# Kernel optimization log

Measured on AMD Instinct MI355X. Metric: run time of the kernel, lower is better.

Reference implementation:

```python
import math
import jax, jax.numpy as jnp
import numpy as np

B = 8
NUM_POINTS = 4096
LATENT = 512
HID = 512
AD = 128
R1, R2, R_ATT = 1.0, 1.5, 0.2
EPS = 1e-5
SQRT_D = math.sqrt(AD)


def _fibonacci_sphere_points(n, radius):
    if n <= 0:
        return np.zeros((0, 3), np.float32)
    i = np.arange(n, dtype=np.float32)
    phi = (1 + 5 ** 0.5) / 2
    theta = 2 * math.pi * i / phi
    z = 1.0 - 2.0 * (i + 0.5) / n
    r_xy = np.sqrt(np.maximum(1.0 - z * z, 0.0))
    return (radius * np.stack((r_xy * np.cos(theta), r_xy * np.sin(theta), z), axis=-1)).astype(np.float32)


def _make_template():
    n_shell = NUM_POINTS - 1
    area_ratio = R1 ** 2 / (R1 ** 2 + R2 ** 2)
    n1 = max(1, round(n_shell * area_ratio))
    n2 = n_shell - n1
    if n2 == 0:
        n1, n2 = n1 - 1, 1
    t1 = _fibonacci_sphere_points(n1, R1)
    t2 = _fibonacci_sphere_points(n2, R2)
    return jnp.asarray(np.concatenate([np.zeros((1, 3), np.float32), t1, t2], axis=0))


def setup_inputs() -> dict:
    key = jax.random.key(0)
    ks = iter(jax.random.split(key, 64))
    d = {}
    d['z'] = jax.random.normal(next(ks), (B, LATENT), jnp.float32)
    d['template'] = _make_template()
    d['wq'] = jax.random.normal(next(ks), (AD, 3), jnp.float32) * 0.1
    d['wk'] = jax.random.normal(next(ks), (AD, 3), jnp.float32) * 0.1
    d['wv'] = jax.random.normal(next(ks), (AD, 3), jnp.float32) * 0.1
    in_dims = [LATENT + 3, LATENT + 3 + AD, LATENT + 3 + AD]
    for s, in_dim in enumerate(in_dims):
        d[f's{s}_w1'] = jax.random.normal(next(ks), (HID, in_dim), jnp.float32) * (1.0 / math.sqrt(in_dim))
        d[f's{s}_b1'] = jnp.zeros((HID,), jnp.float32)
        d[f's{s}_g1'] = jnp.ones((HID,), jnp.float32)
        d[f's{s}_be1'] = jnp.zeros((HID,), jnp.float32)
        d[f's{s}_w2'] = jax.random.normal(next(ks), (HID, HID), jnp.float32) * (1.0 / math.sqrt(HID))
        d[f's{s}_b2'] = jnp.zeros((HID,), jnp.float32)
        d[f's{s}_g2'] = jnp.ones((HID,), jnp.float32)
        d[f's{s}_be2'] = jnp.zeros((HID,), jnp.float32)
        d[f's{s}_w3'] = jax.random.normal(next(ks), (3, HID), jnp.float32) * (1.0 / math.sqrt(HID))
        d[f's{s}_b3'] = jnp.zeros((3,), jnp.float32)
    return d


def _bn_relu(x, gamma, beta):
    # BatchNorm1d in training mode over channel dim of (B, N, C): stats over (B, N)
    mean = jnp.mean(x, axis=(0, 1))
    var = jnp.var(x, axis=(0, 1))
    xn = (x - mean) * jax.lax.rsqrt(var + EPS)
    return jax.nn.relu(xn * gamma + beta)


def _stage(x, w1, b1, g1, be1, w2, b2, g2, be2, w3, b3):
    h = _bn_relu(x @ w1.T + b1, g1, be1)
    h = _bn_relu(h @ w2.T + b2, g2, be2)
    return h @ w3.T + b3


def _local_attention(coords, wq, wk, wv):
    Q = coords @ wq.T  # (B, N, AD)
    K = coords @ wk.T
    V = coords @ wv.T
    sq = jnp.sum(coords * coords, axis=-1)  # (B, N)
    D2 = sq[:, :, None] + sq[:, None, :] - 2.0 * jnp.einsum('bnd,bmd->bnm', coords, coords)
    mask = D2 <= R_ATT ** 2  # diagonal always True (D2=0)
    scores = jnp.einsum('bnd,bmd->bnm', Q, K) / SQRT_D
    scores = jnp.where(mask, scores, -jnp.inf)
    W = jax.nn.softmax(scores, axis=-1)
    W = jnp.where(mask, W, 0.0)
    return jnp.einsum('bnm,bmd->bnd', W, V)


def reference(z, template, wq, wk, wv,
              s0_w1, s0_b1, s0_g1, s0_be1, s0_w2, s0_b2, s0_g2, s0_be2, s0_w3, s0_b3,
              s1_w1, s1_b1, s1_g1, s1_be1, s1_w2, s1_b2, s1_g2, s1_be2, s1_w3, s1_b3,
              s2_w1, s2_b1, s2_g1, s2_be1, s2_w2, s2_b2, s2_g2, s2_be2, s2_w3, s2_b3):
    Bz = z.shape[0]
    z_exp = jnp.broadcast_to(z[:, None, :], (Bz, NUM_POINTS, LATENT))
    tmpl = jnp.broadcast_to(template[None], (Bz, NUM_POINTS, 3))
    coords0 = _stage(jnp.concatenate((z_exp, tmpl), axis=-1),
                     s0_w1, s0_b1, s0_g1, s0_be1, s0_w2, s0_b2, s0_g2, s0_be2, s0_w3, s0_b3)
    attn1 = _local_attention(coords0, wq, wk, wv)
    coords1 = _stage(jnp.concatenate((z_exp, coords0, attn1), axis=-1),
                     s1_w1, s1_b1, s1_g1, s1_be1, s1_w2, s1_b2, s1_g2, s1_be2, s1_w3, s1_b3)
    attn2 = _local_attention(coords1, wq, wk, wv)
    coords2 = _stage(jnp.concatenate((z_exp, coords1, attn2), axis=-1),
                     s2_w1, s2_b1, s2_g1, s2_be1, s2_w2, s2_b2, s2_g2, s2_be2, s2_w3, s2_b3)
    return coords2
```

## Files before the change

### kernel.cpp

```cpp
#include <hip/hip_runtime.h>
#include <math.h>

#define NPTS 4096
#define BATCH 8
#define HIDD 512
#define ROWS 32768
#define R_ATT2 0.04f
#define INV_SQRT_D 0.08838834764831845f

typedef unsigned short u16;
typedef unsigned int u32;
typedef __attribute__((ext_vector_type(8))) short s8v;
typedef __attribute__((ext_vector_type(4))) float f4v;

__device__ __forceinline__ float u2f(u16 v) { return __uint_as_float(((u32)v) << 16); }
__device__ __forceinline__ u16 f2u(float f) {
  u32 u = __float_as_uint(f);
  return (u16)((u + 0x7fffu + ((u >> 16) & 1u)) >> 16);
}
__device__ __forceinline__ u32 packtrunc(float x0, float x1) {
  return (__float_as_uint(x1) & 0xFFFF0000u) | (__float_as_uint(x0) >> 16);
}

__global__ void gram_k(const float* __restrict__ wq, const float* __restrict__ wk,
                       float* __restrict__ G) {
  int ab = threadIdx.x;
  if (ab < 9) {
    int a = ab / 3, b = ab % 3;
    float s = 0.f;
    for (int d = 0; d < 128; ++d) s = fmaf(wq[d * 3 + a], wk[d * 3 + b], s);
    G[ab] = s;
  }
}

__global__ __launch_bounds__(256) void prep2_k(
    const float* __restrict__ z, const float* __restrict__ w1, int ldw,
    const float* __restrict__ b1, const float* __restrict__ w2,
    float* __restrict__ zwbuf, float* __restrict__ ubuf,
    u16* __restrict__ w1abf, u16* __restrict__ w2bf, int doW1a) {
  int wid = blockIdx.x * 4 + (threadIdx.x >> 6);
  int lane = threadIdx.x & 63;
  {
    int b = wid >> 9, c = wid & 511;
    const float* zr = z + b * 512;
    const float* wr = w1 + (size_t)c * ldw;
    float acc = 0.f;
#pragma unroll
    for (int k = lane; k < 512; k += 64) acc = fmaf(zr[k], wr[k], acc);
#pragma unroll
    for (int off = 32; off; off >>= 1) acc += __shfl_down(acc, off);
    if (lane == 0) zwbuf[wid] = acc + b1[c];
  }
  int idx = blockIdx.x * 256 + threadIdx.x;
  if (idx < 1536) {
    int a = idx >> 9, c = idx & 511;
    ubuf[idx] = w1[(size_t)c * ldw + 512 + a];
  }
  if (doW1a && idx < 65536) {
    int n = idx >> 7, k = idx & 127;
    w1abf[idx] = f2u(w1[(size_t)n * 643 + 515 + k]);
  }
  w2bf[idx] = f2u(w2[idx]);
}

__global__ __launch_bounds__(256) void s0l1_k(const float* __restrict__ tmpl,
                                              const float* __restrict__ u,
                                              const float* __restrict__ zw,
                                              u16* __restrict__ h) {
  int wid = blockIdx.x * 4 + (threadIdx.x >> 6);
  int lane = threadIdx.x & 63;
  int b = wid >> 12, n = wid & (NPTS - 1);
  float tx = tmpl[n * 3], ty = tmpl[n * 3 + 1], tz = tmpl[n * 3 + 2];
  int c0 = lane * 8;
  const float* zr = zw + b * 512 + c0;
  const float* u0 = u + c0;
  const float* u1 = u + 512 + c0;
  const float* u2 = u + 1024 + c0;
  u32 outw[4];
#pragma unroll
  for (int t = 0; t < 4; ++t) {
    float v0 = zr[2 * t] + tx * u0[2 * t] + ty * u1[2 * t] + tz * u2[2 * t];
    float v1 = zr[2 * t + 1] + tx * u0[2 * t + 1] + ty * u1[2 * t + 1] + tz * u2[2 * t + 1];
    outw[t] = packtrunc(v0, v1);
  }
  *(uint4*)(h + (size_t)wid * 512 + c0) = *(const uint4*)outw;
}

template <bool MODE1, bool APPLY_A>
__global__ __launch_bounds__(256) void gemm_mfma_k(
    const u16* __restrict__ A, int lda, const u16* __restrict__ B, int ldb, int K,
    const float* __restrict__ bias, const float* __restrict__ zw,
    const float* __restrict__ u, const float4* __restrict__ c4,
    const float* __restrict__ scA, const float* __restrict__ shA,
    u16* __restrict__ C, float* __restrict__ psum, float* __restrict__ psumsq) {
  __shared__ u16 As[128 * 32];
  __shared__ u16 Bs[128 * 32];
  int tid = threadIdx.x;
  int wave = tid >> 6, lane = tid & 63;
  int quad = lane >> 4, l16 = lane & 15;
  int m0 = blockIdx.x * 128, n0 = blockIdx.y * 128;
  int wm = (wave & 1) * 64, wn = (wave >> 1) * 64;
  int srow0 = lane >> 2;
  int sc8 = (lane & 3) * 8;
  f4v acc[4][4];
#pragma unroll
  for (int mi = 0; mi < 4; ++mi)
#pragma unroll
    for (int ni = 0; ni < 4; ++ni) acc[mi][ni] = (f4v){0.f, 0.f, 0.f, 0.f};

  for (int k0 = 0; k0 < K; k0 += 32) {
#pragma unroll
    for (int j = 0; j < 2; ++j) {
      int chunk = wave * 2 + j;
      int row = chunk * 16 + srow0;
      const u16* gA = A + (size_t)(m0 + row) * lda + k0 + sc8;
      const u16* gB = B + (size_t)(n0 + row) * ldb + k0 + sc8;
      if (APPLY_A) {
        uint4 av = *(const uint4*)gA;
        const u16* ap = (const u16*)&av;
        int kb = k0 + sc8;
        u32 outw[4];
#pragma unroll
        for (int t = 0; t < 4; ++t) {
          float x0 = fmaxf(fmaf(u2f(ap[2 * t]), scA[kb + 2 * t], shA[kb + 2 * t]), 0.f);
          float x1 = fmaxf(fmaf(u2f(ap[2 * t + 1]), scA[kb + 2 * t + 1], shA[kb + 2 * t + 1]), 0.f);
          outw[t] = packtrunc(x0, x1);
        }
        *(uint4*)&As[chunk * 512 + srow0 * 32 + sc8] = *(const uint4*)outw;
      } else {
        __builtin_amdgcn_global_load_lds(
            (const __attribute__((address_space(1))) void*)gA,
            (__attribute__((address_space(3))) void*)(As + chunk * 512), 16, 0, 0);
      }
      __builtin_amdgcn_global_load_lds(
          (const __attribute__((address_space(1))) void*)gB,
          (__attribute__((address_space(3))) void*)(Bs + chunk * 512), 16, 0, 0);
    }
    __syncthreads();
    s8v af[4], bfv[4];
#pragma unroll
    for (int mi = 0; mi < 4; ++mi)
      af[mi] = *(const s8v*)&As[(wm + mi * 16 + l16) * 32 + quad * 8];
#pragma unroll
    for (int ni = 0; ni < 4; ++ni)
      bfv[ni] = *(const s8v*)&Bs[(wn + ni * 16 + l16) * 32 + quad * 8];
#pragma unroll
    for (int mi = 0; mi < 4; ++mi)
#pragma unroll
      for (int ni = 0; ni < 4; ++ni)
        acc[mi][ni] = __builtin_amdgcn_mfma_f32_16x16x32_bf16(
            af[mi], bfv[ni], acc[mi][ni], 0, 0, 0);
    __syncthreads();
  }

  int batch = m0 >> 12;
  float e0[4], e1[4], e2[4], e3[4];
  float ps[4] = {0, 0, 0, 0}, pq[4] = {0, 0, 0, 0};
#pragma unroll
  for (int ni = 0; ni < 4; ++ni) {
    int gn = n0 + wn + ni * 16 + l16;
    if (MODE1) {
      e0[ni] = zw[batch * 512 + gn];
      e1[ni] = u[gn];
      e2[ni] = u[512 + gn];
      e3[ni] = u[1024 + gn];
    } else {
      e0[ni] = bias[gn];
    }
  }
#pragma unroll
  for (int mi = 0; mi < 4; ++mi) {
#pragma unroll
    for (int reg = 0; reg < 4; ++reg) {
      int gm = m0 + wm + mi * 16 + quad * 4 + reg;
      float cx = 0.f, cy = 0.f, cz = 0.f;
      if (MODE1) {
        float4 p = c4[gm];
        cx = p.x; cy = p.y; cz = p.z;
      }
#pragma unroll
      for (int ni = 0; ni < 4; ++ni) {
        int gn = n0 + wn + ni * 16 + l16;
        float v = acc[mi][ni][reg] + e0[ni];
        if (MODE1) v += cx * e1[ni] + cy * e2[ni] + cz * e3[ni];
        u16 r = f2u(v);
        C[(size_t)gm * 512 + gn] = r;
        float vr = u2f(r);
        ps[ni] += vr;
        pq[ni] = fmaf(vr, vr, pq[ni]);
      }
    }
  }
  float* Lps = (float*)As;
  float* Lpq = (float*)Bs;
#pragma unroll
  for (int ni = 0; ni < 4; ++ni) {
    Lps[((wave * 4 + quad) * 4 + ni) * 16 + l16] = ps[ni];
    Lpq[((wave * 4 + quad) * 4 + ni) * 16 + l16] = pq[ni];
  }
  __syncthreads();
  if (tid < 128) {
    int wn2 = tid >> 6, rem = tid & 63;
    int nni = rem >> 4, ll = rem & 15;
    int gn = n0 + wn2 * 64 + nni * 16 + ll;
    float s = 0.f, q = 0.f;
#pragma unroll
    for (int wv = 0; wv < 2; ++wv)
#pragma unroll
      for (int qd = 0; qd < 4; ++qd) {
        int w2 = wn2 * 2 + wv;
        s += Lps[((w2 * 4 + qd) * 4 + nni) * 16 + ll];
        q += Lpq[((w2 * 4 + qd) * 4 + nni) * 16 + ll];
      }
    psum[(size_t)blockIdx.x * 512 + gn] = s;
    psumsq[(size_t)blockIdx.x * 512 + gn] = q;
  }
}

__global__ __launch_bounds__(256) void bn_stats_k(const u16* __restrict__ h,
                                                  float* __restrict__ psum,
                                                  float* __restrict__ psumsq) {
  int g = blockIdx.x;
  int c2 = threadIdx.x * 2;
  const u16* base = h + (size_t)g * 16 * 512;
  float s0 = 0, q0 = 0, s1 = 0, q1 = 0;
#pragma unroll
  for (int r = 0; r < 16; ++r) {
    u32 uu = *(const u32*)(base + (size_t)r * 512 + c2);
    float v0 = u2f((u16)(uu & 0xffffu));
    float v1 = u2f((u16)(uu >> 16));
    s0 += v0; q0 += v0 * v0;
    s1 += v1; q1 += v1 * v1;
  }
  psum[g * 512 + c2] = s0; psum[g * 512 + c2 + 1] = s1;
  psumsq[g * 512 + c2] = q0; psumsq[g * 512 + c2 + 1] = q1;
}

__global__ __launch_bounds__(256) void bn_fin_k(
    const float* __restrict__ psum, const float* __restrict__ psumsq, int nslabs,
    const float* __restrict__ gamma, const float* __restrict__ beta,
    float* __restrict__ sc, float* __restrict__ sh) {
  int c = blockIdx.x * 4 + (threadIdx.x >> 6);
  int lane = threadIdx.x & 63;
  float s = 0.f, q = 0.f;
  for (int g = lane; g < nslabs; g += 64) {
    s += psum[g * 512 + c];
    q += psumsq[g * 512 + c];
  }
#pragma unroll
  for (int off = 32; off; off >>= 1) {
    s += __shfl_down(s, off);
    q += __shfl_down(q, off);
  }
  if (lane == 0) {
    float mean = s * (1.f / 32768.f);
    float var = fmaxf(q * (1.f / 32768.f) - mean * mean, 0.f);
    float inv = rsqrtf(var + 1e-5f);
    float scale = gamma[c] * inv;
    sc[c] = scale;
    sh[c] = beta[c] - mean * scale;
  }
}

__global__ __launch_bounds__(256) void l3_k(const u16* __restrict__ h,
                                            const float* __restrict__ sc,
                                            const float* __restrict__ sh,
                                            const float* __restrict__ w3,
                                            const float* __restrict__ b3,
                                            float4* __restrict__ c4out,
                                            float* __restrict__ fout) {
  int wid = blockIdx.x * 4 + (threadIdx.x >> 6);
  int lane = threadIdx.x & 63;
  int k0 = lane * 8;
  uint4 hv = *(const uint4*)(h + (size_t)wid * 512 + k0);
  const u16* hp = (const u16*)&hv;
  float a0 = 0, a1 = 0, a2 = 0;
#pragma unroll
  for (int j = 0; j < 8; ++j) {
    int k = k0 + j;
    float x = fmaxf(fmaf(u2f(hp[j]), sc[k], sh[k]), 0.f);
    a0 = fmaf(x, w3[k], a0);
    a1 = fmaf(x, w3[512 + k], a1);
    a2 = fmaf(x, w3[1024 + k], a2);
  }
#pragma unroll
  for (int off = 32; off; off >>= 1) {
    a0 += __shfl_down(a0, off);
    a1 += __shfl_down(a1, off);
    a2 += __shfl_down(a2, off);
  }
  if (lane == 0) {
    a0 += b3[0]; a1 += b3[1]; a2 += b3[2];
    if (c4out) {
      float sq = a0 * a0 + a1 * a1 + a2 * a2;
      c4out[wid] = make_float4(a0, a1, a2, sq);
    }
    if (fout) {
      fout[(size_t)wid * 3 + 0] = a0;
      fout[(size_t)wid * 3 + 1] = a1;
      fout[(size_t)wid * 3 + 2] = a2;
    }
  }
}

__global__ __launch_bounds__(256) void attn_k(const float4* __restrict__ c4,
                                              const float* __restrict__ G,
                                              const float* __restrict__ wv,
                                              u16* __restrict__ attnb) {
  int wave = threadIdx.x >> 6, lane = threadIdx.x & 63;
  int qbase = (blockIdx.x * 4 + wave) * 4;
  int b = qbase >> 12;
  const float4* cb = c4 + (size_t)b * NPTS;
  float cxq[4], cyq[4], czq[4], thrq[4], g0q[4], g1q[4], g2q[4];
#pragma unroll
  for (int q = 0; q < 4; ++q) {
    float4 cq = c4[qbase + q];
    cxq[q] = cq.x; cyq[q] = cq.y; czq[q] = cq.z;
    thrq[q] = 0.5f * (cq.w - R_ATT2);
    g0q[q] = (cq.x * G[0] + cq.y * G[3] + cq.z * G[6]) * INV_SQRT_D;
    g1q[q] = (cq.x * G[1] + cq.y * G[4] + cq.z * G[7]) * INV_SQRT_D;
    g2q[q] = (cq.x * G[2] + cq.y * G[5] + cq.z * G[8]) * INV_SQRT_D;
  }
  float swq[4] = {0, 0, 0, 0}, sxq[4] = {0, 0, 0, 0};
  float syq[4] = {0, 0, 0, 0}, szq[4] = {0, 0, 0, 0};

  for (int m0 = 0; m0 < NPTS; m0 += 64) {
    float4 p = cb[m0 + lane];
    float hw = 0.5f * p.w;
#pragma unroll
    for (int q = 0; q < 4; ++q) {
      float dot = fmaf(cxq[q], p.x, fmaf(cyq[q], p.y, czq[q] * p.z));
      float s = fmaf(g0q[q], p.x, fmaf(g1q[q], p.y, g2q[q] * p.z));
      float e = (dot >= thrq[q] + hw) ? __expf(s) : 0.f;
      swq[q] += e;
      sxq[q] = fmaf(e, p.x, sxq[q]);
      syq[q] = fmaf(e, p.y, syq[q]);
      szq[q] = fmaf(e, p.z, szq[q]);
    }
  }
#pragma unroll
  for (int q = 0; q < 4; ++q) {
#pragma unroll
    for (int off = 32; off; off >>= 1) {
      swq[q] += __shfl_xor(swq[q], off);
      sxq[q] += __shfl_xor(sxq[q], off);
      syq[q] += __shfl_xor(syq[q], off);
      szq[q] += __shfl_xor(szq[q], off);
    }
  }
  int d0 = lane * 2;
  float w0 = wv[d0 * 3], w1 = wv[d0 * 3 + 1], w2 = wv[d0 * 3 + 2];
  float w3_ = wv[d0 * 3 + 3], w4 = wv[d0 * 3 + 4], w5 = wv[d0 * 3 + 5];
#pragma unroll
  for (int q = 0; q < 4; ++q) {
    float inv = 1.f / swq[q];
    float ox = sxq[q] * inv, oy = syq[q] * inv, oz = szq[q] * inv;
    float v0 = ox * w0 + oy * w1 + oz * w2;
    float v1 = ox * w3_ + oy * w4 + oz * w5;
    u32 pack = (u32)f2u(v0) | ((u32)f2u(v1) << 16);
    *(u32*)(attnb + (size_t)(qbase + q) * 128 + d0) = pack;
  }
}

extern "C" void kernel_launch(void* const* d_in, const int* in_sizes, int n_in,
                              void* d_out, int out_size, void* d_ws, size_t ws_size,
                              hipStream_t stream) {
  const float* z = (const float*)d_in[0];
  const float* tmpl = (const float*)d_in[1];
  const float* wq = (const float*)d_in[2];
  const float* wk = (const float*)d_in[3];
  const float* wv = (const float*)d_in[4];
  const float* sw[3][10];
  for (int s = 0; s < 3; ++s)
    for (int j = 0; j < 10; ++j) sw[s][j] = (const float*)d_in[5 + s * 10 + j];

  char* base = (char*)d_ws;
  size_t off = 0;
  auto alloc = [&](size_t bytes) -> void* {
    void* p = base + off;
    off = (off + bytes + 255) & ~(size_t)255;
    return p;
  };
  u16* hA = (u16*)alloc((size_t)ROWS * 512 * 2);
  u16* hB = (u16*)alloc((size_t)ROWS * 512 * 2);
  u16* attnb = (u16*)alloc((size_t)ROWS * 128 * 2);
  float4* c4 = (float4*)alloc((size_t)ROWS * 16);
  float* psum = (float*)alloc(2048 * 512 * 4);
  float* psumsq = (float*)alloc(2048 * 512 * 4);
  float* zwbuf = (float*)alloc(4096 * 4);
  float* scv = (float*)alloc(512 * 4);
  float* shv = (float*)alloc(512 * 4);
  float* G = (float*)alloc(256);
  u16* w1abf = (u16*)alloc(512 * 128 * 2);
  u16* w2bf = (u16*)alloc(512 * 512 * 2);
  float* ubuf = (float*)alloc(1536 * 4);

  gram_k<<<1, 64, 0, stream>>>(wq, wk, G);

  for (int s = 0; s < 3; ++s) {
    int ldw = (s == 0) ? 515 : 643;
    prep2_k<<<1024, 256, 0, stream>>>(z, sw[s][0], ldw, sw[s][1], sw[s][4],
                                      zwbuf, ubuf, w1abf, w2bf, s == 0 ? 0 : 1);
    if (s == 0) {
      s0l1_k<<<8192, 256, 0, stream>>>(tmpl, ubuf, zwbuf, hA);
      bn_stats_k<<<2048, 256, 0, stream>>>(hA, psum, psumsq);
      bn_fin_k<<<128, 256, 0, stream>>>(psum, psumsq, 2048,
                                        sw[s][2], sw[s][3], scv, shv);
    } else {
      gemm_mfma_k<true, false><<<dim3(256, 4), 256, 0, stream>>>(
          attnb, 128, w1abf, 128, 128, nullptr, zwbuf, ubuf, c4,
          nullptr, nullptr, hA, psum, psumsq);
      bn_fin_k<<<128, 256, 0, stream>>>(psum, psumsq, 256,
                                        sw[s][2], sw[s][3], scv, shv);
    }
    gemm_mfma_k<false, true><<<dim3(256, 4), 256, 0, stream>>>(
        hA, 512, w2bf, 512, 512, sw[s][5], nullptr, nullptr, nullptr,
        scv, shv, hB, psum, psumsq);
    bn_fin_k<<<128, 256, 0, stream>>>(psum, psumsq, 256,
                                      sw[s][6], sw[s][7], scv, shv);
    bool last = (s == 2);
    l3_k<<<8192, 256, 0, stream>>>(hB, scv, shv, sw[s][8], sw[s][9],
                                   last ? nullptr : c4,
                                   last ? (float*)d_out : nullptr);
    if (!last) {
      attn_k<<<2048, 256, 0, stream>>>(c4, G, wv, attnb);
    }
  }
}
```

Baseline: 521.7 us.

## Double GEMM K-step to 64 and skip attention tiles with no neighbors

The GEMM main loop now stages 64 K-elements per iteration in two LDS halves, halving the number of barrier pairs and letting more loads be in flight per sync, at the cost of doubled shared memory per block (possibly lowering occupancy). The local attention loop computes the radius mask first and uses a wave ballot to skip the exp and accumulation work when no lane in a 64-point tile is within range. This exploits spatial sparsity in the neighbor mask but adds a branch and ballot per tile.

```diff
diff --git a/kernel.cpp b/kernel.cpp
--- a/kernel.cpp
+++ b/kernel.cpp
@@ -93,8 +93,10 @@
     const float* __restrict__ u, const float4* __restrict__ c4,
     const float* __restrict__ scA, const float* __restrict__ shA,
     u16* __restrict__ C, float* __restrict__ psum, float* __restrict__ psumsq) {
-  __shared__ u16 As[128 * 32];
-  __shared__ u16 Bs[128 * 32];
+  __shared__ u16 AsL[128 * 32];
+  __shared__ u16 AsH[128 * 32];
+  __shared__ u16 BsL[128 * 32];
+  __shared__ u16 BsH[128 * 32];
   int tid = threadIdx.x;
   int wave = tid >> 6, lane = tid & 63;
   int quad = lane >> 4, l16 = lane & 15;
@@ -108,48 +110,58 @@
 #pragma unroll
     for (int ni = 0; ni < 4; ++ni) acc[mi][ni] = (f4v){0.f, 0.f, 0.f, 0.f};
 
-  for (int k0 = 0; k0 < K; k0 += 32) {
+  for (int k0 = 0; k0 < K; k0 += 64) {
 #pragma unroll
     for (int j = 0; j < 2; ++j) {
       int chunk = wave * 2 + j;
       int row = chunk * 16 + srow0;
-      const u16* gA = A + (size_t)(m0 + row) * lda + k0 + sc8;
-      const u16* gB = B + (size_t)(n0 + row) * ldb + k0 + sc8;
-      if (APPLY_A) {
-        uint4 av = *(const uint4*)gA;
-        const u16* ap = (const u16*)&av;
-        int kb = k0 + sc8;
-        u32 outw[4];
-#pragma unroll
-        for (int t = 0; t < 4; ++t) {
-          float x0 = fmaxf(fmaf(u2f(ap[2 * t]), scA[kb + 2 * t], shA[kb + 2 * t]), 0.f);
-          float x1 = fmaxf(fmaf(u2f(ap[2 * t + 1]), scA[kb + 2 * t + 1], shA[kb + 2 * t + 1]), 0.f);
-          outw[t] = packtrunc(x0, x1);
+#pragma unroll
+      for (int h = 0; h < 2; ++h) {
+        int col = k0 + h * 32 + sc8;
+        u16* As = h ? AsH : AsL;
+        u16* Bs = h ? BsH : BsL;
+        const u16* gA = A + (size_t)(m0 + row) * lda + col;
+        const u16* gB = B + (size_t)(n0 + row) * ldb + col;
+        if (APPLY_A) {
+          uint4 av = *(const uint4*)gA;
+          const u16* ap = (const u16*)&av;
+          u32 outw[4];
+#pragma unroll
+          for (int t = 0; t < 4; ++t) {
+            float x0 = fmaxf(fmaf(u2f(ap[2 * t]), scA[col + 2 * t], shA[col + 2 * t]), 0.f);
+            float x1 = fmaxf(fmaf(u2f(ap[2 * t + 1]), scA[col + 2 * t + 1], shA[col + 2 * t + 1]), 0.f);
+            outw[t] = packtrunc(x0, x1);
+          }
+          *(uint4*)&As[chunk * 512 + srow0 * 32 + sc8] = *(const uint4*)outw;
+        } else {
+          __builtin_amdgcn_global_load_lds(
+              (const __attribute__((address_space(1))) void*)gA,
+              (__attribute__((address_space(3))) void*)(As + chunk * 512), 16, 0, 0);
         }
-        *(uint4*)&As[chunk * 512 + srow0 * 32 + sc8] = *(const uint4*)outw;
-      } else {
         __builtin_amdgcn_global_load_lds(
-            (const __attribute__((address_space(1))) void*)gA,
-            (__attribute__((address_space(3))) void*)(As + chunk * 512), 16, 0, 0);
+            (const __attribute__((address_space(1))) void*)gB,
+            (__attribute__((address_space(3))) void*)(Bs + chunk * 512), 16, 0, 0);
       }
-      __builtin_amdgcn_global_load_lds(
-          (const __attribute__((address_space(1))) void*)gB,
-          (__attribute__((address_space(3))) void*)(Bs + chunk * 512), 16, 0, 0);
     }
     __syncthreads();
-    s8v af[4], bfv[4];
-#pragma unroll
-    for (int mi = 0; mi < 4; ++mi)
-      af[mi] = *(const s8v*)&As[(wm + mi * 16 + l16) * 32 + quad * 8];
-#pragma unroll
-    for (int ni = 0; ni < 4; ++ni)
-      bfv[ni] = *(const s8v*)&Bs[(wn + ni * 16 + l16) * 32 + quad * 8];
-#pragma unroll
-    for (int mi = 0; mi < 4; ++mi)
+#pragma unroll
+    for (int h = 0; h < 2; ++h) {
+      const u16* As = h ? AsH : AsL;
+      const u16* Bs = h ? BsH : BsL;
+      s8v af[4], bfv[4];
+#pragma unroll
+      for (int mi = 0; mi < 4; ++mi)
+        af[mi] = *(const s8v*)&As[(wm + mi * 16 + l16) * 32 + quad * 8];
 #pragma unroll
       for (int ni = 0; ni < 4; ++ni)
-        acc[mi][ni] = __builtin_amdgcn_mfma_f32_16x16x32_bf16(
-            af[mi], bfv[ni], acc[mi][ni], 0, 0, 0);
+        bfv[ni] = *(const s8v*)&Bs[(wn + ni * 16 + l16) * 32 + quad * 8];
+#pragma unroll
+      for (int mi = 0; mi < 4; ++mi)
+#pragma unroll
+        for (int ni = 0; ni < 4; ++ni)
+          acc[mi][ni] = __builtin_amdgcn_mfma_f32_16x16x32_bf16(
+              af[mi], bfv[ni], acc[mi][ni], 0, 0, 0);
+    }
     __syncthreads();
   }
 
@@ -191,8 +203,8 @@
       }
     }
   }
-  float* Lps = (float*)As;
-  float* Lpq = (float*)Bs;
+  float* Lps = (float*)AsL;
+  float* Lpq = (float*)BsL;
 #pragma unroll
   for (int ni = 0; ni < 4; ++ni) {
     Lps[((wave * 4 + quad) * 4 + ni) * 16 + l16] = ps[ni];
@@ -327,15 +339,25 @@
   for (int m0 = 0; m0 < NPTS; m0 += 64) {
     float4 p = cb[m0 + lane];
     float hw = 0.5f * p.w;
+    float dq[4];
+    bool hq[4];
+    bool any = false;
 #pragma unroll
     for (int q = 0; q < 4; ++q) {
-      float dot = fmaf(cxq[q], p.x, fmaf(cyq[q], p.y, czq[q] * p.z));
-      float s = fmaf(g0q[q], p.x, fmaf(g1q[q], p.y, g2q[q] * p.z));
-      float e = (dot >= thrq[q] + hw) ? __expf(s) : 0.f;
-      swq[q] += e;
-      sxq[q] = fmaf(e, p.x, sxq[q]);
-      syq[q] = fmaf(e, p.y, syq[q]);
-      szq[q] = fmaf(e, p.z, szq[q]);
+      dq[q] = fmaf(cxq[q], p.x, fmaf(cyq[q], p.y, czq[q] * p.z));
+      hq[q] = (dq[q] >= thrq[q] + hw);
+      any |= hq[q];
+    }
+    if (__ballot(any)) {
+#pragma unroll
+      for (int q = 0; q < 4; ++q) {
+        float s = fmaf(g0q[q], p.x, fmaf(g1q[q], p.y, g2q[q] * p.z));
+        float e = hq[q] ? __expf(s) : 0.f;
+        swq[q] += e;
+        sxq[q] = fmaf(e, p.x, sxq[q]);
+        syq[q] = fmaf(e, p.y, syq[q]);
+        szq[q] = fmaf(e, p.z, szq[q]);
+      }
     }
   }
 #pragma unroll
```

Result: slower. 555.1 us (+6.4%).
